# Kernel tuning notes

Hardware: AMD Instinct MI355X
Metric: run time of the kernel (lower is better)

The kernel has to match this reference:

```python
import jax, jax.numpy as jnp
import numpy as np

B, S, H, NH = 32, 577, 1024, 16
DH = H // NH


def setup_inputs() -> dict:
    key = jax.random.key(0)
    ks = jax.random.split(key, 10)
    s = 0.02
    return {
        "hidden_states": jax.random.normal(ks[0], (B, S, H), dtype=jnp.float32),
        "attention_mask": jnp.ones((B, S), dtype=jnp.float32),
        "Wq": jax.random.normal(ks[1], (H, H), dtype=jnp.float32) * s,
        "bq": jnp.zeros((H,), dtype=jnp.float32),
        "Wk": jax.random.normal(ks[2], (H, H), dtype=jnp.float32) * s,
        "bk": jnp.zeros((H,), dtype=jnp.float32),
        "Wv": jax.random.normal(ks[3], (H, H), dtype=jnp.float32) * s,
        "bv": jnp.zeros((H,), dtype=jnp.float32),
        "Wo": jax.random.normal(ks[4], (H, H), dtype=jnp.float32) * s,
        "bo": jnp.zeros((H,), dtype=jnp.float32),
    }


def reference(hidden_states, attention_mask, Wq, bq, Wk, bk, Wv, bv, Wo, bo):
    # torch nn.Linear: y = x @ W.T + b
    def heads(x):  # [B,S,H] -> [B,NH,S,DH]
        return x.reshape(B, S, NH, DH).transpose(0, 2, 1, 3)

    q = heads(hidden_states @ Wq.T + bq)
    k = heads(hidden_states @ Wk.T + bk)
    v = heads(hidden_states @ Wv.T + bv)

    scores = jnp.einsum("bhqd,bhkd->bhqk", q, k) / jnp.sqrt(jnp.float32(DH))
    # multiplicative mask, broadcast over heads and query positions
    scores = scores * attention_mask[:, None, None, :]
    probs = jax.nn.softmax(scores, axis=-1)
    ctx = jnp.einsum("bhqk,bhkd->bhqd", probs, v)
    ctx = ctx.transpose(0, 2, 1, 3).reshape(B, S, H)
    return ctx @ Wo.T + bo
```

## Files before the change

### kernel.cpp

```cpp
#include <hip/hip_runtime.h>
#include <hip/hip_bf16.h>


typedef __bf16 bf16_t;
typedef __bf16 bf16x8 __attribute__((ext_vector_type(8)));
typedef __bf16 bf16x4 __attribute__((ext_vector_type(4)));
typedef float f32x4 __attribute__((ext_vector_type(4)));

#define B_   32
#define S_   577
#define SP   608
#define H_   1024
#define NH_  16
#define DH_  64
#define M_   (B_ * S_)

typedef __attribute__((address_space(3))) unsigned int lds_u32;
typedef const __attribute__((address_space(1))) unsigned int glb_u32;
#define STAGE16(gp, lp) __builtin_amdgcn_global_load_lds((glb_u32*)(gp), (lds_u32*)(lp), 16, 0, 0)
#define MFMA_BF16 __builtin_amdgcn_mfma_f32_16x16x32_bf16

__device__ __forceinline__ bf16x8 load8(const bf16_t* p) {
    return *reinterpret_cast<const bf16x8*>(p);
}
__device__ __forceinline__ bf16x8 load8f(const float* p) {
    f32x4 a = *reinterpret_cast<const f32x4*>(p);
    f32x4 b = *reinterpret_cast<const f32x4*>(p + 4);
    bf16x8 r;
    r[0] = (bf16_t)a[0]; r[1] = (bf16_t)a[1]; r[2] = (bf16_t)a[2]; r[3] = (bf16_t)a[3];
    r[4] = (bf16_t)b[0]; r[5] = (bf16_t)b[1]; r[6] = (bf16_t)b[2]; r[7] = (bf16_t)b[3];
    return r;
}

__global__ __launch_bounds__(256) void cvt_f32_bf16(const float* __restrict__ src,
                                                    bf16_t* __restrict__ dst, int n8)
{
    int i = blockIdx.x * blockDim.x + threadIdx.x;
    const int stride = gridDim.x * blockDim.x;
    for (; i < n8; i += stride)
        *reinterpret_cast<bf16x8*>(dst + (size_t)i * 8) = load8f(src + (size_t)i * 8);
}

__global__ __launch_bounds__(256) void cvt_w4(
    const float* __restrict__ s0, const float* __restrict__ s1,
    const float* __restrict__ s2, const float* __restrict__ s3,
    bf16_t* __restrict__ dst)
{
    const int i = blockIdx.x * blockDim.x + threadIdx.x;
    const int which = i >> 17;
    const int off = i & ((1 << 17) - 1);
    const float* s = (which == 0) ? s0 : (which == 1) ? s1 : (which == 2) ? s2 : s3;
    *reinterpret_cast<bf16x8*>(dst + (size_t)i * 8) = load8f(s + (size_t)off * 8);
}

#define AR(par, kk) (((par) * 2 + (kk)) * 8192)
#define BR(par, kk) (32768 + ((par) * 2 + (kk)) * 8192)

#define STG_A(par, kk, T)                                                        \
    do {                                                                         \
        STAGE16(pA0 + (T) * 64 + (kk) * 32, smem + AR(par, kk) + w * 512);       \
        STAGE16(pA1 + (T) * 64 + (kk) * 32, smem + AR(par, kk) + 4096 + w * 512);\
    } while (0)
#define STG_B(par, kk, T)                                                        \
    do {                                                                         \
        STAGE16(pB0 + (T) * 64 + (kk) * 32, smem + BR(par, kk) + w * 512);       \
        STAGE16(pB1 + (T) * 64 + (kk) * 32, smem + BR(par, kk) + 4096 + w * 512);\
    } while (0)

#define PHASE_A(par, kk, STG, SWAP)                                              \
    do {                                                                         \
        asm volatile("s_waitcnt vmcnt(8)" ::: "memory");                         \
        __builtin_amdgcn_s_barrier();                                            \
        STG;                                                                     \
        _Pragma("unroll")                                                        \
        for (int i = 0; i < 8; ++i)                                              \
            af[i] = load8(smem + AR(par, kk) + (wr * 128 + i * 16 + l16) * 32 + quad * 8); \
        bfv[0] = load8(smem + BR(par, kk) + (wc * 64 + l16) * 32 + quad * 8);    \
        bfv[1] = load8(smem + BR(par, kk) + (wc * 64 + 16 + l16) * 32 + quad * 8); \
        __builtin_amdgcn_s_setprio(1);                                           \
        _Pragma("unroll")                                                        \
        for (int i = 0; i < 8; ++i) {                                            \
            acc[i][0] = (SWAP) ? MFMA_BF16(bfv[0], af[i], acc[i][0], 0, 0, 0)    \
                               : MFMA_BF16(af[i], bfv[0], acc[i][0], 0, 0, 0);   \
            acc[i][1] = (SWAP) ? MFMA_BF16(bfv[1], af[i], acc[i][1], 0, 0, 0)    \
                               : MFMA_BF16(af[i], bfv[1], acc[i][1], 0, 0, 0);   \
        }                                                                        \
        __builtin_amdgcn_s_setprio(0);                                           \
    } while (0)

#define PHASE_B(par, kk, STG, SWAP)                                              \
    do {                                                                         \
        STG;                                                                     \
        bfv[2] = load8(smem + BR(par, kk) + (wc * 64 + 32 + l16) * 32 + quad * 8); \
        bfv[3] = load8(smem + BR(par, kk) + (wc * 64 + 48 + l16) * 32 + quad * 8); \
        __builtin_amdgcn_s_setprio(1);                                           \
        _Pragma("unroll")                                                        \
        for (int i = 0; i < 8; ++i) {                                            \
            acc[i][2] = (SWAP) ? MFMA_BF16(bfv[2], af[i], acc[i][2], 0, 0, 0)    \
                               : MFMA_BF16(af[i], bfv[2], acc[i][2], 0, 0, 0);   \
            acc[i][3] = (SWAP) ? MFMA_BF16(bfv[3], af[i], acc[i][3], 0, 0, 0)    \
                               : MFMA_BF16(af[i], bfv[3], acc[i][3], 0, 0, 0);   \
        }                                                                        \
        __builtin_amdgcn_s_setprio(0);                                           \
    } while (0)

#define QKV_MAIN(SWAP)                                                           \
    STG_A(0, 0, 0); STG_B(0, 0, 0); STG_A(0, 1, 0); STG_B(0, 1, 0);              \
    STG_A(1, 0, 1); STG_B(1, 0, 1);                                              \
    for (int it = 0; it < 8; ++it) {                                             \
        const int t1 = 2 * it + 1;                                               \
        const int t2 = (2 * it + 2 < 16) ? 2 * it + 2 : 15;                      \
        const int t3 = (2 * it + 3 < 16) ? 2 * it + 3 : 15;                      \
        PHASE_A(0, 0, STG_A(1, 1, t1), SWAP); PHASE_B(0, 0, STG_B(1, 1, t1), SWAP); \
        PHASE_A(0, 1, STG_A(0, 0, t2), SWAP); PHASE_B(0, 1, STG_B(0, 0, t2), SWAP); \
        PHASE_A(1, 0, STG_A(0, 1, t2), SWAP); PHASE_B(1, 0, STG_B(0, 1, t2), SWAP); \
        PHASE_A(1, 1, STG_A(1, 0, t3), SWAP); PHASE_B(1, 1, STG_B(1, 0, t3), SWAP); \
    }                                                                            \
    asm volatile("s_waitcnt vmcnt(0)" ::: "memory");

__global__ __launch_bounds__(512, 2) void qkv_gemm(
    const bf16_t* __restrict__ Xb,
    const bf16_t* __restrict__ Wqb, const bf16_t* __restrict__ Wkb, const bf16_t* __restrict__ Wvb,
    const float* __restrict__ bq, const float* __restrict__ bk, const float* __restrict__ bv,
    bf16_t* __restrict__ Qb, bf16_t* __restrict__ Kb, bf16_t* __restrict__ VTb)
{
    __shared__ bf16_t smem[65536];
    const int tid  = threadIdx.x;
    const int w    = tid >> 6, lane = tid & 63;
    const int quad = lane >> 4, l16 = lane & 15;
    const int wr = w >> 2, wc = w & 3;

    const int orig = blockIdx.x;
    const int xcd = orig & 7, lin = orig >> 3;
    const int work = (xcd < 4 ? xcd * 110 : 440 + (xcd - 4) * 109) + lin;
    int mt, nt;
    if (work < 864) { const int slab = work / 48, rem = work - slab * 48;
                      nt = rem >> 2; mt = slab * 4 + (rem & 3); }
    else            { nt = work - 864; mt = 72; }
    const int m0 = mt * 256, n0 = nt * 256;

    const int which = n0 >> 10;
    const int nrel0 = n0 & 1023;
    const bf16_t* Wb   = (which == 0) ? Wqb : (which == 1) ? Wkb : Wvb;
    const float*  bias = (which == 0) ? bq  : (which == 1) ? bk  : bv;
    const float   oscale = (which == 0) ? 0.125f : 1.0f;

    const int srow = tid >> 2, scol = (tid & 3) * 8;
    int ga0 = m0 + srow;       if (ga0 > M_ - 1) ga0 = M_ - 1;
    int ga1 = m0 + 128 + srow; if (ga1 > M_ - 1) ga1 = M_ - 1;
    const bf16_t* pA0 = Xb + (size_t)ga0 * H_ + scol;
    const bf16_t* pA1 = Xb + (size_t)ga1 * H_ + scol;
    const bf16_t* pB0 = Wb + (size_t)(nrel0 + srow) * H_ + scol;
    const bf16_t* pB1 = Wb + (size_t)(nrel0 + 128 + srow) * H_ + scol;

    bf16x8 af[8], bfv[4];
    f32x4 acc[8][4] = {};

    if (which != 2) {
        QKV_MAIN(1)
        bf16_t* QKout = (which == 0) ? Qb : Kb;
#pragma unroll
        for (int j = 0; j < 4; ++j) {
            const int nrelj = nrel0 + wc * 64 + j * 16 + quad * 4;
            const int h = nrelj >> 6, d0 = nrelj & 63;
            const f32x4 b4 = *reinterpret_cast<const f32x4*>(&bias[nrelj]);
#pragma unroll
            for (int i = 0; i < 8; ++i) {
                const int m = m0 + wr * 128 + i * 16 + l16;
                if (m >= M_) continue;
                const int b = m / S_, s = m - b * S_;
                const int bh = b * NH_ + h;
                bf16x4 pk;
#pragma unroll
                for (int r = 0; r < 4; ++r) pk[r] = (bf16_t)((acc[i][j][r] + b4[r]) * oscale);
                *reinterpret_cast<bf16x4*>(QKout + ((size_t)bh * S_ + s) * DH_ + d0) = pk;
            }
        }
    } else {
        QKV_MAIN(0)
#pragma unroll
        for (int j = 0; j < 4; ++j) {
            const int nrelj = nrel0 + wc * 64 + j * 16 + l16;
            const int h = nrelj >> 6, d = nrelj & 63;
            const float bv_ = bias[nrelj];
#pragma unroll
            for (int i = 0; i < 8; ++i) {
                const int m = m0 + wr * 128 + i * 16 + quad * 4;
                const int b = m / S_, s = m - b * S_;
                if (m + 3 < M_ && s <= S_ - 4) {
                    bf16x4 pk;
#pragma unroll
                    for (int r = 0; r < 4; ++r) pk[r] = (bf16_t)(acc[i][j][r] + bv_);
                    *reinterpret_cast<bf16x4*>(VTb + ((size_t)(b * NH_ + h) * DH_ + d) * SP + s) = pk;
                } else {
#pragma unroll
                    for (int r = 0; r < 4; ++r) {
                        const int mm = m + r;
                        if (mm >= M_) continue;
                        const int bb = mm / S_, ss = mm - bb * S_;
                        VTb[((size_t)(bb * NH_ + h) * DH_ + d) * SP + ss] = (bf16_t)(acc[i][j][r] + bv_);
                    }
                }
            }
        }
    }
}

__global__ __launch_bounds__(256, 3) void flash_attn(
    const bf16_t* __restrict__ Qb, const bf16_t* __restrict__ Kb,
    const bf16_t* __restrict__ VTb, const float* __restrict__ maskp,
    bf16_t* __restrict__ Ctx)
{
    __shared__ __align__(16) float smask[SP];
    const int tid  = threadIdx.x;
    const int w    = tid >> 6, lane = tid & 63;
    const int quad = lane >> 4, l16 = lane & 15;

    const int bid  = blockIdx.x;
    const int work = (bid & 7) * 320 + (bid >> 3);
    const int bh   = work / 5;
    const int qx   = work - bh * 5;
    const int b    = bh >> 4, h = bh & 15;

    for (int i = tid; i < SP; i += 256)
        smask[i] = (i < S_) ? maskp[b * S_ + i] : 0.f;
    __syncthreads();

    int idx = qx * 4 + w; if (idx > 18) idx = 18;
    const int q0 = idx * 32;

    const bf16_t* Qh = Qb  + (size_t)bh * S_ * DH_;
    const bf16_t* Kh = Kb  + (size_t)bh * S_ * DH_;
    const bf16_t* Vh = VTb + (size_t)bh * DH_ * SP;

    int rqA = q0 + l16;      if (rqA > S_ - 1) rqA = S_ - 1;
    int rqB = q0 + 16 + l16; if (rqB > S_ - 1) rqB = S_ - 1;
    const bf16x8 aqA0 = load8(Qh + rqA * DH_ + quad * 8);
    const bf16x8 aqA1 = load8(Qh + rqA * DH_ + 32 + quad * 8);
    const bf16x8 aqB0 = load8(Qh + rqB * DH_ + quad * 8);
    const bf16x8 aqB1 = load8(Qh + rqB * DH_ + 32 + quad * 8);

    const int g0 = ((l16 >> 2) << 3) + (l16 & 3);
    const int g1 = g0 + 4;

    f32x4 oA[4] = {}, oB[4] = {};
    float lpA = 0.f, lpB = 0.f;

    bf16x8 ka[4], kb_[4];
    {
        int r0 = g0; if (r0 > S_ - 1) r0 = S_ - 1;
        int r1 = g1; if (r1 > S_ - 1) r1 = S_ - 1;
        ka[0] = load8(Kh + r0 * DH_ + quad * 8);
        ka[1] = load8(Kh + r0 * DH_ + 32 + quad * 8);
        ka[2] = load8(Kh + r1 * DH_ + quad * 8);
        ka[3] = load8(Kh + r1 * DH_ + 32 + quad * 8);
    }

    auto body = [&](bf16x8 (&KC)[4], bf16x8 (&KN)[4], const int j0, const bool pf) {
        bf16x8 v0 = load8(Vh + (l16)      * SP + j0 + quad * 8);
        bf16x8 v1 = load8(Vh + (16 + l16) * SP + j0 + quad * 8);
        bf16x8 v2 = load8(Vh + (32 + l16) * SP + j0 + quad * 8);
        bf16x8 v3 = load8(Vh + (48 + l16) * SP + j0 + quad * 8);
        if (pf) {
            int r0 = j0 + 32 + g0; if (r0 > S_ - 1) r0 = S_ - 1;
            int r1 = j0 + 32 + g1; if (r1 > S_ - 1) r1 = S_ - 1;
            KN[0] = load8(Kh + r0 * DH_ + quad * 8);
            KN[1] = load8(Kh + r0 * DH_ + 32 + quad * 8);
            KN[2] = load8(Kh + r1 * DH_ + quad * 8);
            KN[3] = load8(Kh + r1 * DH_ + 32 + quad * 8);
        }
        f32x4 sA0 = {}, sA1 = {}, sB0 = {}, sB1 = {};
        __builtin_amdgcn_s_setprio(1);
        sA0 = MFMA_BF16(KC[0], aqA0, sA0, 0, 0, 0);
        sA0 = MFMA_BF16(KC[1], aqA1, sA0, 0, 0, 0);
        sA1 = MFMA_BF16(KC[2], aqA0, sA1, 0, 0, 0);
        sA1 = MFMA_BF16(KC[3], aqA1, sA1, 0, 0, 0);
        sB0 = MFMA_BF16(KC[0], aqB0, sB0, 0, 0, 0);
        sB0 = MFMA_BF16(KC[1], aqB1, sB0, 0, 0, 0);
        sB1 = MFMA_BF16(KC[2], aqB0, sB1, 0, 0, 0);
        sB1 = MFMA_BF16(KC[3], aqB1, sB1, 0, 0, 0);
        __builtin_amdgcn_s_setprio(0);

        const f32x4 mk0 = *reinterpret_cast<const f32x4*>(&smask[j0 + quad * 8]);
        const f32x4 mk1 = *reinterpret_cast<const f32x4*>(&smask[j0 + quad * 8 + 4]);
        bf16x8 apA, apB;
#pragma unroll
        for (int r = 0; r < 4; ++r) {
            const int c0 = j0 + quad * 8 + r;
            const int c1 = c0 + 4;
            const float eA0 = (c0 < S_) ? __expf(sA0[r] * mk0[r]) : 0.f;
            const float eA1 = (c1 < S_) ? __expf(sA1[r] * mk1[r]) : 0.f;
            const float eB0 = (c0 < S_) ? __expf(sB0[r] * mk0[r]) : 0.f;
            const float eB1 = (c1 < S_) ? __expf(sB1[r] * mk1[r]) : 0.f;
            lpA += eA0 + eA1;
            lpB += eB0 + eB1;
            apA[r] = (bf16_t)eA0; apA[r + 4] = (bf16_t)eA1;
            apB[r] = (bf16_t)eB0; apB[r + 4] = (bf16_t)eB1;
        }
        __builtin_amdgcn_s_setprio(1);
        oA[0] = MFMA_BF16(apA, v0, oA[0], 0, 0, 0);
        oB[0] = MFMA_BF16(apB, v0, oB[0], 0, 0, 0);
        oA[1] = MFMA_BF16(apA, v1, oA[1], 0, 0, 0);
        oB[1] = MFMA_BF16(apB, v1, oB[1], 0, 0, 0);
        oA[2] = MFMA_BF16(apA, v2, oA[2], 0, 0, 0);
        oB[2] = MFMA_BF16(apB, v2, oB[2], 0, 0, 0);
        oA[3] = MFMA_BF16(apA, v3, oA[3], 0, 0, 0);
        oB[3] = MFMA_BF16(apB, v3, oB[3], 0, 0, 0);
        __builtin_amdgcn_s_setprio(0);
    };

    for (int j0 = 0; j0 < S_; j0 += 64) {
        body(ka, kb_, j0, j0 + 32 < S_);
        if (j0 + 32 < S_) body(kb_, ka, j0 + 32, j0 + 64 < S_);
    }

    float lsA = lpA, lsB = lpB;
    lsA += __shfl_xor(lsA, 16); lsA += __shfl_xor(lsA, 32);
    lsB += __shfl_xor(lsB, 16); lsB += __shfl_xor(lsB, 32);
    float livA[4], livB[4];
#pragma unroll
    for (int r = 0; r < 4; ++r) {
        livA[r] = 1.0f / __shfl(lsA, quad * 4 + r);
        livB[r] = 1.0f / __shfl(lsB, quad * 4 + r);
    }

#pragma unroll
    for (int t = 0; t < 4; ++t) {
#pragma unroll
        for (int r = 0; r < 4; ++r) {
            const int sA = q0 + quad * 4 + r;
            const int sB = sA + 16;
            if (sA < S_)
                Ctx[((size_t)(b * S_ + sA) * NH_ + h) * DH_ + t * 16 + l16] =
                    (bf16_t)(oA[t][r] * livA[r]);
            if (sB < S_)
                Ctx[((size_t)(b * S_ + sB) * NH_ + h) * DH_ + t * 16 + l16] =
                    (bf16_t)(oB[t][r] * livB[r]);
        }
    }
}

__global__ __launch_bounds__(256) void out_gemm(
    const bf16_t* __restrict__ Ctx, const bf16_t* __restrict__ Wob,
    const float* __restrict__ bo, float* __restrict__ Out)
{
    __shared__ bf16_t smem[8192];
    bf16_t* sA = smem;
    bf16_t* sB = smem + 4096;
    const int tid  = threadIdx.x;
    const int w    = tid >> 6, lane = tid & 63;
    const int quad = lane >> 4, l16 = lane & 15;
    const int wm = w & 1, wn = w >> 1;

    const int t    = (blockIdx.x & 7) * 145 + (blockIdx.x >> 3);
    const int slab = t / 64;
    const int rem  = t - slab * 64;
    int mt, nt;
    if (slab < 18) { nt = rem >> 3; mt = slab * 8 + (rem & 7); }
    else           { nt = rem;      mt = 144; }
    const int m0 = mt * 128, n0 = nt * 128;

    const int f0 = tid, f1 = 256 + tid;
    const int rA0 = f0 >> 2, cA0 = (f0 & 3) * 8;
    const int rA1 = f1 >> 2, cA1 = (f1 & 3) * 8;
    int ga0 = m0 + rA0; if (ga0 > M_ - 1) ga0 = M_ - 1;
    int ga1 = m0 + rA1; if (ga1 > M_ - 1) ga1 = M_ - 1;
    const bf16_t* pA0 = Ctx + (size_t)ga0 * H_ + cA0;
    const bf16_t* pA1 = Ctx + (size_t)ga1 * H_ + cA1;
    const bf16_t* pB0 = Wob + (size_t)(n0 + rA0) * H_ + cA0;
    const bf16_t* pB1 = Wob + (size_t)(n0 + rA1) * H_ + cA1;
    bf16_t* lA0 = sA + w * 512;
    bf16_t* lA1 = sA + 2048 + w * 512;
    bf16_t* lB0 = sB + w * 512;
    bf16_t* lB1 = sB + 2048 + w * 512;

    f32x4 acc[4][4] = {};
    for (int k0 = 0; k0 < H_; k0 += 32) {
        STAGE16(pA0 + k0, lA0);
        STAGE16(pA1 + k0, lA1);
        STAGE16(pB0 + k0, lB0);
        STAGE16(pB1 + k0, lB1);
        __syncthreads();
        bf16x8 af[4], bfv[4];
#pragma unroll
        for (int tt = 0; tt < 4; ++tt) {
            af[tt]  = load8(sA + (wm * 64 + tt * 16 + l16) * 32 + quad * 8);
            bfv[tt] = load8(sB + (wn * 64 + tt * 16 + l16) * 32 + quad * 8);
        }
#pragma unroll
        for (int i = 0; i < 4; ++i)
#pragma unroll
            for (int j = 0; j < 4; ++j)
                acc[i][j] = MFMA_BF16(bfv[j], af[i], acc[i][j], 0, 0, 0);
        __syncthreads();
    }

#pragma unroll
    for (int j = 0; j < 4; ++j) {
        const int nb = n0 + wn * 64 + j * 16 + quad * 4;
        const f32x4 b4 = *reinterpret_cast<const f32x4*>(&bo[nb]);
#pragma unroll
        for (int i = 0; i < 4; ++i) {
            const int m = m0 + wm * 64 + i * 16 + l16;
            if (m >= M_) continue;
            f32x4 v = acc[i][j] + b4;
            *reinterpret_cast<f32x4*>(Out + (size_t)m * H_ + nb) = v;
        }
    }
}

extern "C" void kernel_launch(void* const* d_in, const int* in_sizes, int n_in,
                              void* d_out, int out_size, void* d_ws, size_t ws_size,
                              hipStream_t stream) {
    const float* hidden = (const float*)d_in[0];
    const float* mask   = (const float*)d_in[1];
    const float* Wq = (const float*)d_in[2];
    const float* bq = (const float*)d_in[3];
    const float* Wk = (const float*)d_in[4];
    const float* bk = (const float*)d_in[5];
    const float* Wv = (const float*)d_in[6];
    const float* bv = (const float*)d_in[7];
    const float* Wo = (const float*)d_in[8];
    const float* bo = (const float*)d_in[9];
    float* out = (float*)d_out;

    const size_t QK_EL = (size_t)B_ * NH_ * S_ * DH_;
    const size_t VT_EL = (size_t)B_ * NH_ * SP * DH_;
    const size_t X_EL  = (size_t)M_ * H_;
    const size_t W_EL  = (size_t)H_ * H_;
    const size_t NEED  = (2 * QK_EL + VT_EL + X_EL + 4 * W_EL) * sizeof(bf16_t);
    if (ws_size < NEED) {
        hipMemsetAsync(d_out, 0, (size_t)out_size * sizeof(float), stream);
        return;
    }

    bf16_t* ws    = (bf16_t*)d_ws;
    bf16_t* Qb    = ws;
    bf16_t* Kb    = Qb + QK_EL;
    bf16_t* VTb   = Kb + QK_EL;
    bf16_t* XbCtx = VTb + VT_EL;
    bf16_t* Wqb   = XbCtx + X_EL;
    bf16_t* Wkb   = Wqb + W_EL;
    bf16_t* Wvb   = Wkb + W_EL;
    bf16_t* Wob   = Wvb + W_EL;

    cvt_f32_bf16<<<2048, 256, 0, stream>>>(hidden, XbCtx, (int)(X_EL / 8));
    cvt_w4<<<2048, 256, 0, stream>>>(Wq, Wk, Wv, Wo, Wqb);

    qkv_gemm<<<dim3(876), dim3(512), 0, stream>>>(XbCtx, Wqb, Wkb, Wvb, bq, bk, bv, Qb, Kb, VTb);

    flash_attn<<<dim3(2560), dim3(256), 0, stream>>>(Qb, Kb, VTb, mask, XbCtx);

    out_gemm<<<dim3(1160), dim3(256), 0, stream>>>(XbCtx, Wob, bo, out);
}
```

Measured before the change: 511.5 us.

## Restructure QKV GEMM into double-buffered tiles with XOR-swizzled LDS reads

Replaces the four-stage parity/k-half rotation of the QKV GEMM main loop with a two-buffer scheme. Each 64-wide K tile is consumed from one buffer while the next tile is staged into the other, with extra barriers between LDS reads and MFMA groups. It also XOR-swizzles the column that each thread stages and reads, to cut LDS bank conflicts on the fragment loads. The extra barriers and shallower prefetch depth (one tile ahead instead of more) may expose more global-load latency.

```diff
diff --git a/kernel.cpp b/kernel.cpp
--- a/kernel.cpp
+++ b/kernel.cpp
@@ -53,68 +53,70 @@
     *reinterpret_cast<bf16x8*>(dst + (size_t)i * 8) = load8f(s + (size_t)off * 8);
 }
 
-#define AR(par, kk) (((par) * 2 + (kk)) * 8192)
-#define BR(par, kk) (32768 + ((par) * 2 + (kk)) * 8192)
-
-#define STG_A(par, kk, T)                                                        \
+#define AR(buf, kh) (((buf) * 2 + (kh)) * 8192)
+#define BR(buf, kh) (32768 + ((buf) * 2 + (kh)) * 8192)
+
+#define STG_A(buf, kh, T)                                                        \
     do {                                                                         \
-        STAGE16(pA0 + (T) * 64 + (kk) * 32, smem + AR(par, kk) + w * 512);       \
-        STAGE16(pA1 + (T) * 64 + (kk) * 32, smem + AR(par, kk) + 4096 + w * 512);\
+        STAGE16(pA0 + (T) * 64 + (kh) * 32, smem + AR(buf, kh) + w * 512);       \
+        STAGE16(pA1 + (T) * 64 + (kh) * 32, smem + AR(buf, kh) + 4096 + w * 512);\
     } while (0)
-#define STG_B(par, kk, T)                                                        \
+#define STG_B(buf, kh, T)                                                        \
     do {                                                                         \
-        STAGE16(pB0 + (T) * 64 + (kk) * 32, smem + BR(par, kk) + w * 512);       \
-        STAGE16(pB1 + (T) * 64 + (kk) * 32, smem + BR(par, kk) + 4096 + w * 512);\
+        STAGE16(pB0 + (T) * 64 + (kh) * 32, smem + BR(buf, kh) + w * 512);       \
+        STAGE16(pB1 + (T) * 64 + (kh) * 32, smem + BR(buf, kh) + 4096 + w * 512);\
     } while (0)
 
-#define PHASE_A(par, kk, STG, SWAP)                                              \
+#define RD_A(buf, kh)                                                            \
+    do { _Pragma("unroll")                                                       \
+        for (int i = 0; i < 8; ++i)                                              \
+            af[i] = load8(smem + AR(buf, kh) + (wr * 128 + i * 16 + l16) * 32 + rdsw); \
+    } while (0)
+#define RD_B(buf, kh, j)                                                         \
+    bfv[j] = load8(smem + BR(buf, kh) + (wc * 64 + (j) * 16 + l16) * 32 + rdsw)
+
+#define MM(jj, SWAP)                                                             \
     do {                                                                         \
-        asm volatile("s_waitcnt vmcnt(8)" ::: "memory");                         \
-        __builtin_amdgcn_s_barrier();                                            \
-        STG;                                                                     \
-        _Pragma("unroll")                                                        \
-        for (int i = 0; i < 8; ++i)                                              \
-            af[i] = load8(smem + AR(par, kk) + (wr * 128 + i * 16 + l16) * 32 + quad * 8); \
-        bfv[0] = load8(smem + BR(par, kk) + (wc * 64 + l16) * 32 + quad * 8);    \
-        bfv[1] = load8(smem + BR(par, kk) + (wc * 64 + 16 + l16) * 32 + quad * 8); \
         __builtin_amdgcn_s_setprio(1);                                           \
         _Pragma("unroll")                                                        \
         for (int i = 0; i < 8; ++i) {                                            \
-            acc[i][0] = (SWAP) ? MFMA_BF16(bfv[0], af[i], acc[i][0], 0, 0, 0)    \
-                               : MFMA_BF16(af[i], bfv[0], acc[i][0], 0, 0, 0);   \
-            acc[i][1] = (SWAP) ? MFMA_BF16(bfv[1], af[i], acc[i][1], 0, 0, 0)    \
-                               : MFMA_BF16(af[i], bfv[1], acc[i][1], 0, 0, 0);   \
+            acc[i][jj]     = (SWAP) ? MFMA_BF16(bfv[jj], af[i], acc[i][jj], 0, 0, 0)     \
+                                    : MFMA_BF16(af[i], bfv[jj], acc[i][jj], 0, 0, 0);    \
+            acc[i][jj + 1] = (SWAP) ? MFMA_BF16(bfv[jj + 1], af[i], acc[i][jj + 1], 0, 0, 0) \
+                                    : MFMA_BF16(af[i], bfv[jj + 1], acc[i][jj + 1], 0, 0, 0);\
         }                                                                        \
         __builtin_amdgcn_s_setprio(0);                                           \
     } while (0)
 
-#define PHASE_B(par, kk, STG, SWAP)                                              \
+#define VMB4 do { asm volatile("s_waitcnt vmcnt(4)" ::: "memory");               \
+                  __builtin_amdgcn_s_barrier(); } while (0)
+#define BAR  __builtin_amdgcn_s_barrier()
+
+#define TILE(CUR, T, TS, SWAP)                                                   \
     do {                                                                         \
-        STG;                                                                     \
-        bfv[2] = load8(smem + BR(par, kk) + (wc * 64 + 32 + l16) * 32 + quad * 8); \
-        bfv[3] = load8(smem + BR(par, kk) + (wc * 64 + 48 + l16) * 32 + quad * 8); \
-        __builtin_amdgcn_s_setprio(1);                                           \
-        _Pragma("unroll")                                                        \
-        for (int i = 0; i < 8; ++i) {                                            \
-            acc[i][2] = (SWAP) ? MFMA_BF16(bfv[2], af[i], acc[i][2], 0, 0, 0)    \
-                               : MFMA_BF16(af[i], bfv[2], acc[i][2], 0, 0, 0);   \
-            acc[i][3] = (SWAP) ? MFMA_BF16(bfv[3], af[i], acc[i][3], 0, 0, 0)    \
-                               : MFMA_BF16(af[i], bfv[3], acc[i][3], 0, 0, 0);   \
-        }                                                                        \
-        __builtin_amdgcn_s_setprio(0);                                           \
+        VMB4;                                                                    \
+        RD_A(CUR, 0); RD_B(CUR, 0, 0); RD_B(CUR, 0, 1);                          \
+        STG_A(CUR ^ 1, 0, TS);                                                   \
+        BAR; MM(0, SWAP);                                                        \
+        RD_B(CUR, 0, 2); RD_B(CUR, 0, 3);                                        \
+        STG_B(CUR ^ 1, 0, TS);                                                   \
+        BAR; MM(2, SWAP);                                                        \
+        VMB4;                                                                    \
+        RD_A(CUR, 1); RD_B(CUR, 1, 0); RD_B(CUR, 1, 1);                          \
+        STG_A(CUR ^ 1, 1, TS);                                                   \
+        BAR; MM(0, SWAP);                                                        \
+        RD_B(CUR, 1, 2); RD_B(CUR, 1, 3);                                        \
+        STG_B(CUR ^ 1, 1, TS);                                                   \
+        BAR; MM(2, SWAP);                                                        \
     } while (0)
 
 #define QKV_MAIN(SWAP)                                                           \
     STG_A(0, 0, 0); STG_B(0, 0, 0); STG_A(0, 1, 0); STG_B(0, 1, 0);              \
-    STG_A(1, 0, 1); STG_B(1, 0, 1);                                              \
     for (int it = 0; it < 8; ++it) {                                             \
-        const int t1 = 2 * it + 1;                                               \
-        const int t2 = (2 * it + 2 < 16) ? 2 * it + 2 : 15;                      \
-        const int t3 = (2 * it + 3 < 16) ? 2 * it + 3 : 15;                      \
-        PHASE_A(0, 0, STG_A(1, 1, t1), SWAP); PHASE_B(0, 0, STG_B(1, 1, t1), SWAP); \
-        PHASE_A(0, 1, STG_A(0, 0, t2), SWAP); PHASE_B(0, 1, STG_B(0, 0, t2), SWAP); \
-        PHASE_A(1, 0, STG_A(0, 1, t2), SWAP); PHASE_B(1, 0, STG_B(0, 1, t2), SWAP); \
-        PHASE_A(1, 1, STG_A(1, 0, t3), SWAP); PHASE_B(1, 1, STG_B(1, 0, t3), SWAP); \
+        const int t0 = 2 * it, t1 = 2 * it + 1;                                  \
+        const int s0 = t1, s1 = (t1 + 1 < 16) ? t1 + 1 : 15;                     \
+        TILE(0, t0, s0, SWAP);                                                   \
+        TILE(1, t1, s1, SWAP);                                                   \
     }                                                                            \
     asm volatile("s_waitcnt vmcnt(0)" ::: "memory");
 
@@ -129,6 +131,7 @@
     const int w    = tid >> 6, lane = tid & 63;
     const int quad = lane >> 4, l16 = lane & 15;
     const int wr = w >> 2, wc = w & 3;
+    const int rdsw = (quad ^ (l16 & 3)) * 8;
 
     const int orig = blockIdx.x;
     const int xcd = orig & 7, lin = orig >> 3;
@@ -145,7 +148,8 @@
     const float*  bias = (which == 0) ? bq  : (which == 1) ? bk  : bv;
     const float   oscale = (which == 0) ? 0.125f : 1.0f;
 
-    const int srow = tid >> 2, scol = (tid & 3) * 8;
+    const int srow = tid >> 2;
+    const int scol = (((tid & 3) ^ ((tid >> 2) & 3))) * 8;
     int ga0 = m0 + srow;       if (ga0 > M_ - 1) ga0 = M_ - 1;
     int ga1 = m0 + 128 + srow; if (ga1 > M_ - 1) ga1 = M_ - 1;
     const bf16_t* pA0 = Xb + (size_t)ga0 * H_ + scol;
```

Measured after the change: 514.8 us. About the same (+0.7%).
